# Kernel tuning notes

Hardware: AMD Instinct MI355X
Metric: run time of the kernel (lower is better)

## Reference

```python
import jax, jax.numpy as jnp
import numpy as np

HIDDEN = 2048
HEADS = 16
HEAD_DIM = HIDDEN // HEADS  # 128
B, S = 2, 2048


def setup_inputs() -> dict:
    key = jax.random.key(0)
    ks = jax.random.split(key, 9)
    s_in = 1.0 / np.sqrt(HIDDEN)
    return {
        "X": jax.random.normal(ks[0], (B, S, HIDDEN), dtype=jnp.float32),
        "attention_mask": jnp.ones((B, S, S), dtype=jnp.int32),
        "Wq": jax.random.uniform(ks[1], (HIDDEN, HIDDEN), jnp.float32, -s_in, s_in),
        "bq": jax.random.uniform(ks[2], (HIDDEN,), jnp.float32, -s_in, s_in),
        "Wk": jax.random.uniform(ks[3], (HIDDEN, HEAD_DIM), jnp.float32, -s_in, s_in),
        "bk": jax.random.uniform(ks[4], (HEAD_DIM,), jnp.float32, -s_in, s_in),
        "Wv": jax.random.uniform(ks[5], (HIDDEN, HEAD_DIM), jnp.float32, -s_in, s_in),
        "bv": jax.random.uniform(ks[6], (HEAD_DIM,), jnp.float32, -s_in, s_in),
        "Wo": jax.random.uniform(ks[7], (HIDDEN, HIDDEN), jnp.float32, -s_in, s_in),
        "bo": jax.random.uniform(ks[8], (HIDDEN,), jnp.float32, -s_in, s_in),
    }


def reference(X, attention_mask, Wq, bq, Wk, bk, Wv, bv, Wo, bo):
    b, s, _ = X.shape
    # Projections
    Q = X @ Wq + bq                      # (B, S, H*D)
    K = X @ Wk + bk                      # (B, S, D)  shared across heads (MQA)
    V = X @ Wv + bv                      # (B, S, D)
    Q = Q.reshape(b, s, HEADS, HEAD_DIM).transpose(0, 2, 1, 3)  # (B, H, S, D)
    scale = 1.0 / jnp.sqrt(jnp.float32(HEAD_DIM))
    # QK^T with shared K head
    scores = jnp.einsum('bhqd,bkd->bhqk', Q, K) * scale          # (B, H, S, S)
    scores = jnp.where(attention_mask[:, None, :, :] == 0, -jnp.inf, scores)
    attn = jax.nn.softmax(scores, axis=-1)
    # dropout_rate = 0.0 (eval) -> identity
    out = jnp.einsum('bhqk,bkd->bhqd', attn, V)                  # (B, H, S, D)
    out = out.transpose(0, 2, 1, 3).reshape(b, s, HIDDEN)        # (B, S, hidden)
    return out @ Wo + bo
```

## Files before the change

kernel.cpp:

```cpp
#include <hip/hip_runtime.h>
#include <cstdint>
#include <cstddef>

#define HIDDEN 2048
#define HEADS 16
#define HD 128
#define BSZ 2
#define SEQ 2048
#define MTOT (BSZ * SEQ)
#define NQKV (HIDDEN + 2 * HD)
#define SL2E 0.12751743f

typedef unsigned short ushort_t;
typedef __attribute__((ext_vector_type(8))) __bf16 bf16x8;
typedef __attribute__((ext_vector_type(4))) float f32x4;
typedef __attribute__((ext_vector_type(16))) float f32x16;

typedef __attribute__((address_space(3))) unsigned int as3_u32;
typedef __attribute__((address_space(1))) const unsigned int as1_u32;

__device__ __forceinline__ ushort_t f2bf(float x) {
  union { float f; unsigned u; } v; v.f = x;
  unsigned r = v.u + 0x7fffu + ((v.u >> 16) & 1u);
  return (ushort_t)(r >> 16);
}
__device__ __forceinline__ unsigned pk_bf16(float a, float b) {
  union { float f; unsigned u; } x, y; x.f = a; y.f = b;
  return (x.u >> 16) | (y.u & 0xFFFF0000u);
}

__device__ __forceinline__ void gld16(const void* g, void* lds) {
  __builtin_amdgcn_global_load_lds((as1_u32*)g, (as3_u32*)lds, 16, 0, 0);
}

__global__ __launch_bounds__(256) void cvt_bf16_kernel(
    const float* __restrict__ in, ushort_t* __restrict__ out, int n4) {
  int i = blockIdx.x * 256 + threadIdx.x;
  if (i >= n4) return;
  float4 v = ((const float4*)in)[i];
  ushort4 o;
  o.x = f2bf(v.x); o.y = f2bf(v.y); o.z = f2bf(v.z); o.w = f2bf(v.w);
  ((ushort4*)out)[i] = o;
}

__global__ __launch_bounds__(256) void cvtT_qkv_kernel(
    const float* __restrict__ Wq, const float* __restrict__ Wk,
    const float* __restrict__ Wv, ushort_t* __restrict__ WT) {
  __shared__ float tile[32][36];
  const int t = threadIdx.x;
  const int nb = blockIdx.x * 32, kb = blockIdx.y * 32;
  const float* W; int N, nc; float scale;
  if (nb < HIDDEN)            { W = Wq; N = HIDDEN; nc = nb;               scale = SL2E; }
  else if (nb < HIDDEN + HD)  { W = Wk; N = HD;     nc = nb - HIDDEN;      scale = 1.f; }
  else                        { W = Wv; N = HD;     nc = nb - HIDDEN - HD; scale = 1.f; }
  {
    int row = t >> 3, c4 = (t & 7) << 2;
    float4 v = *(const float4*)(W + (size_t)(kb + row) * N + nc + c4);
    tile[row][c4] = v.x * scale; tile[row][c4 + 1] = v.y * scale;
    tile[row][c4 + 2] = v.z * scale; tile[row][c4 + 3] = v.w * scale;
  }
  __syncthreads();
  {
    int nl = t >> 3, k4 = (t & 7) << 2;
    ushort4 o;
    o.x = f2bf(tile[k4 + 0][nl]); o.y = f2bf(tile[k4 + 1][nl]);
    o.z = f2bf(tile[k4 + 2][nl]); o.w = f2bf(tile[k4 + 3][nl]);
    *(ushort4*)(WT + (size_t)(nb + nl) * HIDDEN + kb + k4) = o;
  }
}

__global__ __launch_bounds__(256) void cvtT_kernel(
    const float* __restrict__ W, ushort_t* __restrict__ WT, int K, int N) {
  __shared__ float tile[32][36];
  const int t = threadIdx.x;
  const int kb = blockIdx.y * 32, nb = blockIdx.x * 32;
  {
    int row = t >> 3, c4 = (t & 7) << 2;
    float4 v = *(const float4*)(W + (size_t)(kb + row) * N + nb + c4);
    tile[row][c4] = v.x; tile[row][c4 + 1] = v.y;
    tile[row][c4 + 2] = v.z; tile[row][c4 + 3] = v.w;
  }
  __syncthreads();
  {
    int nl = t >> 3, k4 = (t & 7) << 2;
    ushort4 o;
    o.x = f2bf(tile[k4 + 0][nl]); o.y = f2bf(tile[k4 + 1][nl]);
    o.z = f2bf(tile[k4 + 2][nl]); o.w = f2bf(tile[k4 + 3][nl]);
    *(ushort4*)(WT + (size_t)(nb + nl) * K + kb + k4) = o;
  }
}

__global__ __launch_bounds__(256) void transpose_v_kernel(
    const ushort_t* __restrict__ Vin, ushort_t* __restrict__ Vt) {
  __shared__ ushort_t tile[32][40];
  const int t = threadIdx.x;
  const int rb = blockIdx.x * 32, cb = blockIdx.y * 32;
  {
    int row = t >> 3, c4 = (t & 7) << 2;
    ushort4 v = *(const ushort4*)(Vin + (size_t)(rb + row) * NQKV + cb + c4);
    tile[row][c4] = v.x; tile[row][c4 + 1] = v.y;
    tile[row][c4 + 2] = v.z; tile[row][c4 + 3] = v.w;
  }
  __syncthreads();
  {
    int dl = t >> 3, r4 = (t & 7) << 2;
    ushort4 o;
    o.x = tile[r4 + 0][dl]; o.y = tile[r4 + 1][dl];
    o.z = tile[r4 + 2][dl]; o.w = tile[r4 + 3][dl];
    *(ushort4*)(Vt + (size_t)(cb + dl) * MTOT + rb + r4) = o;
  }
}

__global__ void concat_bias_kernel(const float* __restrict__ bq,
                                   const float* __restrict__ bk,
                                   const float* __restrict__ bv,
                                   float* __restrict__ o) {
  int i = blockIdx.x * 256 + threadIdx.x;
  if (i >= NQKV) return;
  o[i] = (i < HIDDEN) ? bq[i] * SL2E
       : (i < HIDDEN + HD ? bk[i - HIDDEN] : bv[i - HIDDEN - HD]);
}

__global__ __launch_bounds__(256) void mask_flags_kernel(
    const int* __restrict__ mask, int* __restrict__ flags) {
  const int kt = blockIdx.x, qt = blockIdx.y, b = blockIdx.z;
  const int t = threadIdx.x;
  int allv = 1, anyv = 0;
  const size_t base = (size_t)b * SEQ * SEQ + (size_t)qt * 128 * SEQ + kt * 64;
  for (int i = t; i < 2048; i += 256) {
    const int row = i >> 4, c4 = (i & 15) << 2;
    const int4 v = *(const int4*)(mask + base + (size_t)row * SEQ + c4);
    const int nz = (v.x != 0) & (v.y != 0) & (v.z != 0) & (v.w != 0);
    const int nzany = (v.x != 0) | (v.y != 0) | (v.z != 0) | (v.w != 0);
    allv &= nz; anyv |= nzany;
  }
  const int wAll = __all(allv), wAny = __any(anyv);
  __shared__ int sA[4], sO[4];
  if ((t & 63) == 0) { sA[t >> 6] = wAll; sO[t >> 6] = wAny; }
  __syncthreads();
  if (t == 0) {
    const int A = sA[0] & sA[1] & sA[2] & sA[3];
    const int O = sO[0] | sO[1] | sO[2] | sO[3];
    flags[(b * 16 + qt) * 32 + kt] = A ? 2 : (O ? 1 : 0);
  }
}

template <int OUTF32>
__global__ __launch_bounds__(256) void gemm_mfma(
    const ushort_t* __restrict__ A, const ushort_t* __restrict__ Bt,
    const float* __restrict__ bias, void* __restrict__ C,
    int M, int N, int K, int nm_per_xcd) {
  __shared__ ushort_t As[2][128 * 64];
  __shared__ ushort_t Bs[2][128 * 64];
  const int t = threadIdx.x;
  const int w = t >> 6, l = t & 63;
  const int id = blockIdx.x;
  const int xcd = id & 7, j = id >> 3;
  const int mt = xcd * nm_per_xcd + (j % nm_per_xcd);
  const int nt = j / nm_per_xcd;
  const int mb = mt * 128, nb = nt * 128;
  const int wm = (w >> 1) * 64, wn = (w & 1) * 64;
  const int fl = l & 15, g = l >> 4;
  const int srow = l >> 3, cphys = l & 7;

  f32x4 acc[4][4];
#pragma unroll
  for (int i = 0; i < 4; ++i)
#pragma unroll
    for (int jj = 0; jj < 4; ++jj) acc[i][jj] = (f32x4){0.f, 0.f, 0.f, 0.f};

#pragma unroll
  for (int jj = 0; jj < 4; ++jj) {
    const int inst = w * 4 + jj;
    const int row = inst * 8 + srow;
    const int clog = cphys ^ (row & 7);
    gld16(A + (size_t)(mb + row) * K + clog * 8, &As[0][inst * 512]);
    gld16(Bt + (size_t)(nb + row) * K + clog * 8, &Bs[0][inst * 512]);
  }

  int cur = 0;
  for (int k0 = 0; k0 < K; k0 += 64) {
    __syncthreads();
    if (k0 + 64 < K) {
#pragma unroll
      for (int jj = 0; jj < 4; ++jj) {
        const int inst = w * 4 + jj;
        const int row = inst * 8 + srow;
        const int clog = cphys ^ (row & 7);
        gld16(A + (size_t)(mb + row) * K + k0 + 64 + clog * 8,
              &As[cur ^ 1][inst * 512]);
        gld16(Bt + (size_t)(nb + row) * K + k0 + 64 + clog * 8,
              &Bs[cur ^ 1][inst * 512]);
      }
    }
    const ushort_t* Ac = &As[cur][0];
    const ushort_t* Bc = &Bs[cur][0];
#pragma unroll
    for (int s = 0; s < 2; ++s) {
      bf16x8 af[4], bfr[4];
#pragma unroll
      for (int i = 0; i < 4; ++i) {
        const int m = wm + i * 16 + fl;
        af[i] = *(const bf16x8*)&Ac[m * 64 + (((s << 2) + g) ^ (m & 7)) * 8];
        const int n = wn + i * 16 + fl;
        bfr[i] = *(const bf16x8*)&Bc[n * 64 + (((s << 2) + g) ^ (n & 7)) * 8];
      }
#pragma unroll
      for (int i = 0; i < 4; ++i)
#pragma unroll
        for (int jj = 0; jj < 4; ++jj)
          acc[i][jj] = __builtin_amdgcn_mfma_f32_16x16x32_bf16(
              af[i], bfr[jj], acc[i][jj], 0, 0, 0);
    }
    cur ^= 1;
  }

#pragma unroll
  for (int jj = 0; jj < 4; ++jj) {
    const int col = nb + wn + jj * 16 + fl;
    const float bv = bias[col];
#pragma unroll
    for (int i = 0; i < 4; ++i) {
      const int row0 = mb + wm + i * 16 + g * 4;
#pragma unroll
      for (int r = 0; r < 4; ++r) {
        const float val = acc[i][jj][r] + bv;
        if (OUTF32)
          ((float*)C)[(size_t)(row0 + r) * N + col] = val;
        else
          ((ushort_t*)C)[(size_t)(row0 + r) * N + col] = f2bf(val);
      }
    }
  }
}

__global__ __launch_bounds__(256, 2) void flash_mfma(
    const ushort_t* __restrict__ QKV,
    const ushort_t* __restrict__ Vt,
    const int* __restrict__ mask,
    const int* __restrict__ flags,
    ushort_t* __restrict__ Ab)
{
  __shared__ ushort_t Kbuf[2][64 * 128];
  __shared__ ushort_t Vbuf[2][64 * 128];

  const int qt = blockIdx.x, h = blockIdx.y, b = blockIdx.z;
  const int t = threadIdx.x, w = t >> 6, l = t & 63;
  const int q31 = l & 31, hi = l >> 5;
  const int qbase = qt * 128;
  const int qrow = qbase + w * 32 + q31;

  bf16x8 qf[8];
#pragma unroll
  for (int ks = 0; ks < 8; ++ks)
    qf[ks] = *(const bf16x8*)(QKV + (size_t)(b * SEQ + qrow) * NQKV + h * HD +
                              ks * 16 + hi * 8);

  bf16x8 onesf;
  {
    const ushort_t ov = (q31 == 0) ? (ushort_t)0x3F80 : (ushort_t)0;
#pragma unroll
    for (int jj = 0; jj < 8; ++jj) ((ushort_t*)&onesf)[jj] = ov;
  }

#pragma unroll
  for (int j = 0; j < 4; ++j) {
    const int inst = w * 4 + j;
    const int krow = inst * 4 + (l >> 4);
    const int ck = (l & 15) ^ (krow & 15);
    gld16(QKV + (size_t)(b * SEQ + krow) * NQKV + HIDDEN + ck * 8,
          &Kbuf[0][inst * 512]);
    const int vr = inst * 4 + (l >> 4);
    const int clog = (l & 15) ^ (vr & 15);
    const int d = 2 * vr + (clog >> 3);
    gld16(Vt + (size_t)d * MTOT + b * SEQ + (clog & 7) * 8,
          &Vbuf[0][inst * 512]);
  }

  const size_t mbase = (size_t)b * SEQ * SEQ;

  f32x16 oacc[4], lacc;
#pragma unroll
  for (int d = 0; d < 4; ++d)
#pragma unroll
    for (int r = 0; r < 16; ++r) oacc[d][r] = 0.f;
#pragma unroll
  for (int r = 0; r < 16; ++r) lacc[r] = 0.f;

  int cur = 0;
  for (int kt = 0; kt < SEQ / 64; ++kt) {
    const int kbase = kt * 64;
    const int flag = flags[((b * 16 + qt) << 5) + kt];
    __syncthreads();

    {
      const int knb = (kt + 1 < SEQ / 64) ? (kbase + 64) : kbase;
#pragma unroll
      for (int j = 0; j < 4; ++j) {
        const int inst = w * 4 + j;
        const int krow = inst * 4 + (l >> 4);
        const int ck = (l & 15) ^ (krow & 15);
        gld16(QKV + (size_t)(b * SEQ + knb + krow) * NQKV + HIDDEN + ck * 8,
              &Kbuf[cur ^ 1][inst * 512]);
        const int vr = inst * 4 + (l >> 4);
        const int clog = (l & 15) ^ (vr & 15);
        const int d = 2 * vr + (clog >> 3);
        gld16(Vt + (size_t)d * MTOT + b * SEQ + knb + (clog & 7) * 8,
              &Vbuf[cur ^ 1][inst * 512]);
      }
    }

    const ushort_t* Kc = &Kbuf[cur][0];
    f32x16 sc[2];
#pragma unroll
    for (int kk = 0; kk < 2; ++kk)
#pragma unroll
      for (int r = 0; r < 16; ++r) sc[kk][r] = 0.f;

    __builtin_amdgcn_s_setprio(1);
#pragma unroll
    for (int ks = 0; ks < 8; ++ks)
#pragma unroll
      for (int kk = 0; kk < 2; ++kk) {
        const int key = kk * 32 + q31;
        const bf16x8 kf = *(const bf16x8*)&Kc[key * 128 +
                                              (((ks << 1) + hi) ^ (key & 15)) * 8];
        sc[kk] = __builtin_amdgcn_mfma_f32_32x32x16_bf16(kf, qf[ks], sc[kk],
                                                         0, 0, 0);
      }
    __builtin_amdgcn_s_setprio(0);

    if (flag != 2) {
#pragma unroll
      for (int kk = 0; kk < 2; ++kk)
#pragma unroll
        for (int r = 0; r < 16; ++r) {
          const int key = kbase + kk * 32 + (r & 3) + ((r >> 2) << 3) + (hi << 2);
          if (!mask[mbase + (size_t)qrow * SEQ + key]) sc[kk][r] = -1e30f;
        }
    }

    bf16x8 pa[4];
#pragma unroll
    for (int kk = 0; kk < 2; ++kk) {
      float pv[16];
#pragma unroll
      for (int r = 0; r < 16; ++r) pv[r] = __builtin_amdgcn_exp2f(sc[kk][r]);
#pragma unroll
      for (int half = 0; half < 2; ++half) {
        const int bs = half * 8;
        unsigned a0 = pk_bf16(pv[bs + 0], pv[bs + 1]);
        unsigned a1 = pk_bf16(pv[bs + 2], pv[bs + 3]);
        unsigned b0 = pk_bf16(pv[bs + 4], pv[bs + 5]);
        unsigned b1 = pk_bf16(pv[bs + 6], pv[bs + 7]);
        asm("v_permlane32_swap_b32 %0, %1" : "+v"(a0), "+v"(b0));
        asm("v_permlane32_swap_b32 %0, %1" : "+v"(a1), "+v"(b1));
        union { unsigned u[4]; bf16x8 v; } uu;
        uu.u[0] = a0; uu.u[1] = a1; uu.u[2] = b0; uu.u[3] = b1;
        pa[kk * 2 + half] = uu.v;
      }
    }

    const ushort_t* Vc = &Vbuf[cur][0];
    __builtin_amdgcn_s_setprio(1);
#pragma unroll
    for (int ks = 0; ks < 4; ++ks) {
#pragma unroll
      for (int dt = 0; dt < 4; ++dt) {
        const int d = dt * 32 + q31;
        const int vr = d >> 1;
        const int clog = ((d & 1) << 3) + (ks << 1) + hi;
        const bf16x8 vf =
            *(const bf16x8*)&Vc[vr * 128 + (clog ^ (vr & 15)) * 8];
        oacc[dt] = __builtin_amdgcn_mfma_f32_32x32x16_bf16(pa[ks], vf,
                                                           oacc[dt], 0, 0, 0);
      }
      lacc = __builtin_amdgcn_mfma_f32_32x32x16_bf16(pa[ks], onesf, lacc,
                                                     0, 0, 0);
    }
    __builtin_amdgcn_s_setprio(0);
    cur ^= 1;
  }

#pragma unroll
  for (int r = 0; r < 16; ++r) {
    const float ls = __shfl(lacc[r], l & 32, 64);
    const float invl = 1.0f / ls;
    const int row = b * SEQ + qbase + w * 32 + (r & 3) + ((r >> 2) << 3) +
                    (hi << 2);
#pragma unroll
    for (int dt = 0; dt < 4; ++dt)
      Ab[(size_t)row * HIDDEN + h * HD + dt * 32 + q31] =
          f2bf(oacc[dt][r] * invl);
  }
}

extern "C" void kernel_launch(void* const* d_in, const int* in_sizes, int n_in,
                              void* d_out, int out_size, void* d_ws, size_t ws_size,
                              hipStream_t stream) {
  const float* X  = (const float*)d_in[0];
  const int* mask = (const int*)d_in[1];
  const float* Wq = (const float*)d_in[2];
  const float* bq = (const float*)d_in[3];
  const float* Wk = (const float*)d_in[4];
  const float* bk = (const float*)d_in[5];
  const float* Wv = (const float*)d_in[6];
  const float* bv = (const float*)d_in[7];
  const float* Wo = (const float*)d_in[8];
  const float* bo = (const float*)d_in[9];
  float* out = (float*)d_out;

  char* p = (char*)d_ws;
  ushort_t* QKVb = (ushort_t*)p; p += (size_t)MTOT * NQKV * 2;
  ushort_t* Xb   = (ushort_t*)p; p += (size_t)MTOT * HIDDEN * 2;
  ushort_t* WT   = (ushort_t*)p; p += (size_t)NQKV * HIDDEN * 2;
  ushort_t* WoT  = (ushort_t*)p; p += (size_t)HIDDEN * HIDDEN * 2;
  ushort_t* Vt   = (ushort_t*)p; p += (size_t)HD * MTOT * 2;
  float* biasQKV = (float*)p;    p += 4096;
  int* flags     = (int*)p;      p += BSZ * 16 * 32 * 4;
  ushort_t* Ab = Xb;

  cvt_bf16_kernel<<<(MTOT * HIDDEN / 4 + 255) / 256, 256, 0, stream>>>(
      X, Xb, MTOT * HIDDEN / 4);
  cvtT_qkv_kernel<<<dim3(NQKV / 32, HIDDEN / 32), 256, 0, stream>>>(
      Wq, Wk, Wv, WT);
  cvtT_kernel<<<dim3(HIDDEN / 32, HIDDEN / 32), 256, 0, stream>>>(
      Wo, WoT, HIDDEN, HIDDEN);
  concat_bias_kernel<<<(NQKV + 255) / 256, 256, 0, stream>>>(bq, bk, bv, biasQKV);
  mask_flags_kernel<<<dim3(32, 16, BSZ), 256, 0, stream>>>(mask, flags);

  gemm_mfma<0><<<dim3((MTOT / 128) * (NQKV / 128)), 256, 0, stream>>>(
      Xb, WT, biasQKV, QKVb, MTOT, NQKV, HIDDEN, (MTOT / 128) / 8);
  transpose_v_kernel<<<dim3(MTOT / 32, HD / 32), 256, 0, stream>>>(
      QKVb + HIDDEN + HD, Vt);
  flash_mfma<<<dim3(SEQ / 128, HEADS, BSZ), 256, 0, stream>>>(
      QKVb, Vt, mask, flags, Ab);
  gemm_mfma<1><<<dim3((MTOT / 128) * (HIDDEN / 128)), 256, 0, stream>>>(
      Ab, WoT, bo, out, MTOT, HIDDEN, HIDDEN, (MTOT / 128) / 8);
}
```

Baseline: 339.4 us.

## Replace GEMM with 256x256-tile 8-wave ping-pong MFMA kernel

Replaces the 128x128, 4-wave double-buffered GEMM with a 256x256-tile, 512-thread kernel used for both the QKV and output projections. The main loop is split into four sub-phases, each loading a slice of fragments from LDS and running one MFMA block. Each phase also issues a global-to-LDS prefetch, and phases are separated by explicit s_barrier, waitcnt and setprio calls. The aim is to overlap memory traffic with matrix math and double per-block data reuse. In exchange the grid shrinks to 144 and 128 blocks, fewer than the CU count, and each block uses about 128KB of LDS, so occupancy and CU coverage may suffer.

```diff
diff --git a/kernel.cpp b/kernel.cpp
--- a/kernel.cpp
+++ b/kernel.cpp
@@ -31,6 +31,12 @@
 
 __device__ __forceinline__ void gld16(const void* g, void* lds) {
   __builtin_amdgcn_global_load_lds((as1_u32*)g, (as3_u32*)lds, 16, 0, 0);
+}
+
+__device__ __forceinline__ void barf() {
+  asm volatile("" ::: "memory");
+  __builtin_amdgcn_s_barrier();
+  asm volatile("" ::: "memory");
 }
 
 __global__ __launch_bounds__(256) void cvt_bf16_kernel(
@@ -146,85 +152,169 @@
 }
 
 template <int OUTF32>
-__global__ __launch_bounds__(256) void gemm_mfma(
+__global__ __launch_bounds__(512, 2) void gemm_mfma8(
     const ushort_t* __restrict__ A, const ushort_t* __restrict__ Bt,
     const float* __restrict__ bias, void* __restrict__ C,
     int M, int N, int K, int nm_per_xcd) {
-  __shared__ ushort_t As[2][128 * 64];
-  __shared__ ushort_t Bs[2][128 * 64];
+  __shared__ ushort_t As[2][256 * 64];
+  __shared__ ushort_t Bs[2][256 * 64];
   const int t = threadIdx.x;
   const int w = t >> 6, l = t & 63;
   const int id = blockIdx.x;
-  const int xcd = id & 7, j = id >> 3;
-  const int mt = xcd * nm_per_xcd + (j % nm_per_xcd);
-  const int nt = j / nm_per_xcd;
-  const int mb = mt * 128, nb = nt * 128;
-  const int wm = (w >> 1) * 64, wn = (w & 1) * 64;
+  const int xcd = id & 7, jb = id >> 3;
+  const int mt = xcd * nm_per_xcd + (jb % nm_per_xcd);
+  const int nt = jb / nm_per_xcd;
+  const int mb = mt * 256, nb = nt * 256;
+  const int wm = (w >> 2) * 128, wn = (w & 3) * 64;
   const int fl = l & 15, g = l >> 4;
-  const int srow = l >> 3, cphys = l & 7;
-
-  f32x4 acc[4][4];
-#pragma unroll
-  for (int i = 0; i < 4; ++i)
-#pragma unroll
-    for (int jj = 0; jj < 4; ++jj) acc[i][jj] = (f32x4){0.f, 0.f, 0.f, 0.f};
-
-#pragma unroll
-  for (int jj = 0; jj < 4; ++jj) {
-    const int inst = w * 4 + jj;
-    const int row = inst * 8 + srow;
-    const int clog = cphys ^ (row & 7);
-    gld16(A + (size_t)(mb + row) * K + clog * 8, &As[0][inst * 512]);
-    gld16(Bt + (size_t)(nb + row) * K + clog * 8, &Bs[0][inst * 512]);
-  }
-
-  int cur = 0;
-  for (int k0 = 0; k0 < K; k0 += 64) {
-    __syncthreads();
-    if (k0 + 64 < K) {
-#pragma unroll
-      for (int jj = 0; jj < 4; ++jj) {
-        const int inst = w * 4 + jj;
-        const int row = inst * 8 + srow;
-        const int clog = cphys ^ (row & 7);
-        gld16(A + (size_t)(mb + row) * K + k0 + 64 + clog * 8,
-              &As[cur ^ 1][inst * 512]);
-        gld16(Bt + (size_t)(nb + row) * K + k0 + 64 + clog * 8,
-              &Bs[cur ^ 1][inst * 512]);
-      }
-    }
-    const ushort_t* Ac = &As[cur][0];
-    const ushort_t* Bc = &Bs[cur][0];
-#pragma unroll
-    for (int s = 0; s < 2; ++s) {
-      bf16x8 af[4], bfr[4];
+  const int srow = l >> 3;
+  const int clog = (l & 7) ^ (srow & 7);
+  const int ntile = K >> 6;
+
+  auto stageA = [&](int s, int half, int kt) {
+    const int rr = half * 128 + w * 16;
+    for (int jj = 0; jj < 2; ++jj)
+      gld16(A + (size_t)(mb + rr + jj * 8 + srow) * K + kt * 64 + clog * 8,
+            &As[s][(rr + jj * 8) * 64]);
+  };
+  auto stageB = [&](int s, int half, int kt) {
+    const int rr = half * 128 + w * 16;
+    for (int jj = 0; jj < 2; ++jj)
+      gld16(Bt + (size_t)(nb + rr + jj * 8 + srow) * K + kt * 64 + clog * 8,
+            &Bs[s][(rr + jj * 8) * 64]);
+  };
+
+  f32x4 acc[8][4];
+#pragma unroll
+  for (int i = 0; i < 8; ++i)
+#pragma unroll
+    for (int jf = 0; jf < 4; ++jf) acc[i][jf] = (f32x4){0.f, 0.f, 0.f, 0.f};
+
+  stageB(0, 0, 0); stageB(0, 1, 0);
+  stageA(0, 0, 0); stageA(0, 1, 0);
+  stageB(1, 0, 1); stageB(1, 1, 1);
+  asm volatile("s_waitcnt vmcnt(4)" ::: "memory");
+  barf();
+
+  for (int it = 0; it < ntile / 2; ++it) {
+    const int kb2 = 2 * it + 1;
+    int kc = 2 * it + 2; if (kc >= ntile) kc = ntile - 1;
+    int kd = 2 * it + 3; if (kd >= ntile) kd = ntile - 1;
+
+    bf16x8 af[4][2], b0[2][2], b1[2][2];
+
+#pragma unroll
+    for (int h = 0; h < 2; ++h) {
+      const ushort_t* Ac = As[h];
+      const ushort_t* Bc = Bs[h];
+
 #pragma unroll
       for (int i = 0; i < 4; ++i) {
         const int m = wm + i * 16 + fl;
-        af[i] = *(const bf16x8*)&Ac[m * 64 + (((s << 2) + g) ^ (m & 7)) * 8];
-        const int n = wn + i * 16 + fl;
-        bfr[i] = *(const bf16x8*)&Bc[n * 64 + (((s << 2) + g) ^ (n & 7)) * 8];
-      }
+#pragma unroll
+        for (int s2 = 0; s2 < 2; ++s2)
+          af[i][s2] =
+              *(const bf16x8*)&Ac[m * 64 + (((s2 << 2) + g) ^ (fl & 7)) * 8];
+      }
+#pragma unroll
+      for (int jf = 0; jf < 2; ++jf) {
+        const int n = wn + jf * 16 + fl;
+#pragma unroll
+        for (int s2 = 0; s2 < 2; ++s2)
+          b0[jf][s2] =
+              *(const bf16x8*)&Bc[n * 64 + (((s2 << 2) + g) ^ (fl & 7)) * 8];
+      }
+      if (h == 0) stageA(1, 0, kb2); else stageA(0, 0, kc);
+      barf();
+      asm volatile("s_waitcnt lgkmcnt(0)" ::: "memory");
+      __builtin_amdgcn_sched_barrier(0);
+      __builtin_amdgcn_s_setprio(1);
 #pragma unroll
       for (int i = 0; i < 4; ++i)
 #pragma unroll
-        for (int jj = 0; jj < 4; ++jj)
-          acc[i][jj] = __builtin_amdgcn_mfma_f32_16x16x32_bf16(
-              af[i], bfr[jj], acc[i][jj], 0, 0, 0);
+        for (int jf = 0; jf < 2; ++jf)
+#pragma unroll
+          for (int s2 = 0; s2 < 2; ++s2)
+            acc[i][jf] = __builtin_amdgcn_mfma_f32_16x16x32_bf16(
+                af[i][s2], b0[jf][s2], acc[i][jf], 0, 0, 0);
+      __builtin_amdgcn_s_setprio(0);
+      barf();
+
+#pragma unroll
+      for (int jf = 0; jf < 2; ++jf) {
+        const int n = wn + (2 + jf) * 16 + fl;
+#pragma unroll
+        for (int s2 = 0; s2 < 2; ++s2)
+          b1[jf][s2] =
+              *(const bf16x8*)&Bc[n * 64 + (((s2 << 2) + g) ^ (fl & 7)) * 8];
+      }
+      if (h == 0) stageA(1, 1, kb2); else stageA(0, 1, kc);
+      barf();
+      asm volatile("s_waitcnt lgkmcnt(0)" ::: "memory");
+      __builtin_amdgcn_sched_barrier(0);
+      __builtin_amdgcn_s_setprio(1);
+#pragma unroll
+      for (int i = 0; i < 4; ++i)
+#pragma unroll
+        for (int jf = 0; jf < 2; ++jf)
+#pragma unroll
+          for (int s2 = 0; s2 < 2; ++s2)
+            acc[i][2 + jf] = __builtin_amdgcn_mfma_f32_16x16x32_bf16(
+                af[i][s2], b1[jf][s2], acc[i][2 + jf], 0, 0, 0);
+      __builtin_amdgcn_s_setprio(0);
+      barf();
+
+#pragma unroll
+      for (int i = 0; i < 4; ++i) {
+        const int m = wm + (4 + i) * 16 + fl;
+#pragma unroll
+        for (int s2 = 0; s2 < 2; ++s2)
+          af[i][s2] =
+              *(const bf16x8*)&Ac[m * 64 + (((s2 << 2) + g) ^ (fl & 7)) * 8];
+      }
+      if (h == 0) stageB(0, 0, kc); else stageB(1, 0, kd);
+      barf();
+      asm volatile("s_waitcnt lgkmcnt(0)" ::: "memory");
+      __builtin_amdgcn_sched_barrier(0);
+      __builtin_amdgcn_s_setprio(1);
+#pragma unroll
+      for (int i = 0; i < 4; ++i)
+#pragma unroll
+        for (int jf = 0; jf < 2; ++jf)
+#pragma unroll
+          for (int s2 = 0; s2 < 2; ++s2)
+            acc[4 + i][2 + jf] = __builtin_amdgcn_mfma_f32_16x16x32_bf16(
+                af[i][s2], b1[jf][s2], acc[4 + i][2 + jf], 0, 0, 0);
+      __builtin_amdgcn_s_setprio(0);
+      barf();
+
+      if (h == 0) stageB(0, 1, kc); else stageB(1, 1, kd);
+      asm volatile("s_waitcnt vmcnt(4)" ::: "memory");
+      barf();
+      __builtin_amdgcn_s_setprio(1);
+#pragma unroll
+      for (int i = 0; i < 4; ++i)
+#pragma unroll
+        for (int jf = 0; jf < 2; ++jf)
+#pragma unroll
+          for (int s2 = 0; s2 < 2; ++s2)
+            acc[4 + i][jf] = __builtin_amdgcn_mfma_f32_16x16x32_bf16(
+                af[i][s2], b0[jf][s2], acc[4 + i][jf], 0, 0, 0);
+      __builtin_amdgcn_s_setprio(0);
+      barf();
     }
-    cur ^= 1;
-  }
-
-#pragma unroll
-  for (int jj = 0; jj < 4; ++jj) {
-    const int col = nb + wn + jj * 16 + fl;
+  }
+
+#pragma unroll
+  for (int jf = 0; jf < 4; ++jf) {
+    const int col = nb + wn + jf * 16 + fl;
     const float bv = bias[col];
 #pragma unroll
-    for (int i = 0; i < 4; ++i) {
+    for (int i = 0; i < 8; ++i) {
       const int row0 = mb + wm + i * 16 + g * 4;
 #pragma unroll
       for (int r = 0; r < 4; ++r) {
-        const float val = acc[i][jj][r] + bv;
+        const float val = acc[i][jf][r] + bv;
         if (OUTF32)
           ((float*)C)[(size_t)(row0 + r) * N + col] = val;
         else
@@ -429,12 +519,12 @@
   concat_bias_kernel<<<(NQKV + 255) / 256, 256, 0, stream>>>(bq, bk, bv, biasQKV);
   mask_flags_kernel<<<dim3(32, 16, BSZ), 256, 0, stream>>>(mask, flags);
 
-  gemm_mfma<0><<<dim3((MTOT / 128) * (NQKV / 128)), 256, 0, stream>>>(
-      Xb, WT, biasQKV, QKVb, MTOT, NQKV, HIDDEN, (MTOT / 128) / 8);
+  gemm_mfma8<0><<<dim3((MTOT / 256) * (NQKV / 256)), 512, 0, stream>>>(
+      Xb, WT, biasQKV, QKVb, MTOT, NQKV, HIDDEN, (MTOT / 256) / 8);
   transpose_v_kernel<<<dim3(MTOT / 32, HD / 32), 256, 0, stream>>>(
       QKVb + HIDDEN + HD, Vt);
   flash_mfma<<<dim3(SEQ / 128, HEADS, BSZ), 256, 0, stream>>>(
       QKVb, Vt, mask, flags, Ab);
-  gemm_mfma<1><<<dim3((MTOT / 128) * (HIDDEN / 128)), 256, 0, stream>>>(
-      Ab, WoT, bo, out, MTOT, HIDDEN, HIDDEN, (MTOT / 128) / 8);
-}
+  gemm_mfma8<1><<<dim3((MTOT / 256) * (HIDDEN / 256)), 512, 0, stream>>>(
+      Ab, WoT, bo, out, MTOT, HIDDEN, HIDDEN, (MTOT / 256) / 8);
+}
```

Result: slower. 350.2 us (+3.2%).
